# Kernel optimization log

Measured on AMD Instinct MI355X. Metric: run time of the kernel, lower is better.

The kernel has to match this reference:

```python
import jax, jax.numpy as jnp
import numpy as np

N_NODES = 100_000
N_EDGES = 1_000_000
IN_FTS = 64
EDGE_IN_FTS = 64
OUT_DIM = 64
LN_EPS = 1e-5


def setup_inputs() -> dict:
    key = jax.random.key(0)
    ks = jax.random.split(key, 9)
    def lin(k, fan_in, fan_out):
        bound = 1.0 / np.sqrt(fan_in)
        kw, kb = jax.random.split(k)
        W = jax.random.uniform(kw, (fan_out, fan_in), jnp.float32, -bound, bound)
        b = jax.random.uniform(kb, (fan_out,), jnp.float32, -bound, bound)
        return W, b
    node_fts = jax.random.normal(ks[0], (N_NODES, IN_FTS), jnp.float32)
    edge_fts = jax.random.normal(ks[1], (N_EDGES, EDGE_IN_FTS), jnp.float32)
    edges = jax.random.randint(ks[2], (2, N_EDGES), 0, N_NODES, jnp.int64)
    W_init, b_init = lin(ks[3], EDGE_IN_FTS, OUT_DIM)
    W_mlp, b_mlp = lin(ks[4], 2 * IN_FTS + OUT_DIM, OUT_DIM)
    W_alpha, b_alpha = lin(ks[5], 2 * IN_FTS + OUT_DIM, 1)
    return {
        "node_fts": node_fts, "edge_fts": edge_fts, "edges": edges,
        "W_init": W_init, "b_init": b_init,
        "W_mlp": W_mlp, "b_mlp": b_mlp,
        "W_alpha": W_alpha, "b_alpha": b_alpha,
    }


def _layer_norm(x):
    # F.layer_norm over last dim, no affine params
    m = jnp.mean(x, axis=-1, keepdims=True)
    v = jnp.mean(jnp.square(x - m), axis=-1, keepdims=True)
    return (x - m) * jax.lax.rsqrt(v + LN_EPS)


def reference(node_fts, edge_fts, edges, W_init, b_init, W_mlp, b_mlp, W_alpha, b_alpha):
    # initial edge projection: [E, edge_in] -> [E, out_dim]
    e = edge_fts @ W_init.T + b_init
    # gather head/tail node features: [E, in_fts] each
    head_vectors = jnp.take(node_fts, edges[0], axis=0)
    tail_vectors = jnp.take(node_fts, edges[1], axis=0)
    combined = jnp.concatenate([e, head_vectors, tail_vectors], axis=1)  # [E, 2*in+out]
    alpha = jax.nn.sigmoid(combined @ W_alpha.T + b_alpha)  # [E, 1]
    processed = jnp.tanh(combined @ W_mlp.T + b_mlp)        # [E, out_dim]
    right_side = _layer_norm(processed) * alpha
    return _layer_norm(e + right_side)
```

## Files before the change

### kernel.cpp

```cpp
#include <hip/hip_runtime.h>
#include <hip/hip_bf16.h>

typedef __bf16 bf16;
typedef bf16 bf16x8 __attribute__((ext_vector_type(8)));
typedef float f32x4 __attribute__((ext_vector_type(4)));

#define MFMA16(a, b, c) __builtin_amdgcn_mfma_f32_16x16x32_bf16((a), (b), (c), 0, 0, 0)

__device__ __forceinline__ float fast_rcp(float x) { return __builtin_amdgcn_rcpf(x); }
__device__ __forceinline__ float fast_rsq(float x) { return __builtin_amdgcn_rsqf(x); }
__device__ __forceinline__ float fast_tanh(float x) {
    float e = __expf(2.0f * x);
    return 1.0f - 2.0f * fast_rcp(e + 1.0f);
}
__device__ __forceinline__ float fast_sigmoid(float x) {
    return fast_rcp(1.0f + __expf(-x));
}

__device__ __forceinline__ bf16x8 cvt8(const float* __restrict__ p) {
    f32x4 a = *(const f32x4*)p;
    f32x4 b = *(const f32x4*)(p + 4);
    bf16x8 r;
    r[0] = (bf16)a[0]; r[1] = (bf16)a[1]; r[2] = (bf16)a[2]; r[3] = (bf16)a[3];
    r[4] = (bf16)b[0]; r[5] = (bf16)b[1]; r[6] = (bf16)b[2]; r[7] = (bf16)b[3];
    return r;
}

#define WS_WAF  8192
#define WS_BMF  8320
#define WS_BAF  8576

__global__ void fuse_weights_kernel(const float* __restrict__ W_init,
                                    const float* __restrict__ b_init,
                                    const float* __restrict__ W_mlp,
                                    const float* __restrict__ b_mlp,
                                    const float* __restrict__ W_alpha,
                                    const float* __restrict__ b_alpha,
                                    char* __restrict__ ws)
{
    bf16*  Wf  = (bf16*)ws;
    bf16*  waf = (bf16*)(ws + WS_WAF);
    float* bMf = (float*)(ws + WS_BMF);
    float* bAf = (float*)(ws + WS_BAF);
    const int idx = blockIdx.x * 256 + threadIdx.x;
    if (idx < 4096) {
        const int o = idx >> 6, k = idx & 63;
        float acc = 0.f;
        for (int j = 0; j < 64; ++j)
            acc += W_mlp[o * 192 + j] * W_init[j * 64 + k];
        Wf[o * 64 + k] = (bf16)acc;
    } else if (idx < 4160) {
        const int o = idx - 4096;
        float acc = b_mlp[o];
        for (int j = 0; j < 64; ++j)
            acc += W_mlp[o * 192 + j] * b_init[j];
        bMf[o] = acc;
    } else if (idx < 4224) {
        const int k = idx - 4160;
        float acc = 0.f;
        for (int j = 0; j < 64; ++j)
            acc += W_alpha[j] * W_init[j * 64 + k];
        waf[k] = (bf16)acc;
    } else if (idx == 4224) {
        float acc = b_alpha[0];
        for (int j = 0; j < 64; ++j)
            acc += W_alpha[j] * b_init[j];
        bAf[0] = acc;
    }
}

__global__ __launch_bounds__(256, 3)
void edge_update_kernel(const float* __restrict__ node_fts,
                        const float* __restrict__ edge_fts,
                        const int*   __restrict__ edges,
                        const float* __restrict__ W_init,
                        const float* __restrict__ b_init,
                        const float* __restrict__ W_mlp,
                        const float* __restrict__ W_alpha,
                        const char*  __restrict__ ws,
                        float* __restrict__ out,
                        int E)
{
    __shared__ bf16 sW2[64][200];
    __shared__ bf16 sWa[224];

    const int tid  = threadIdx.x;
    const int lane = tid & 63;
    const int wv   = tid >> 6;
    const int n    = lane & 15;
    const int q    = lane >> 4;

    const bf16*  Wf  = (const bf16*)ws;
    const bf16*  waf = (const bf16*)(ws + WS_WAF);
    const float* bMf = (const float*)(ws + WS_BMF);
    const float* bAf = (const float*)(ws + WS_BAF);

    for (int c = tid; c < 64 * 24; c += 256) {
        const int r = c / 24;
        const int o = (c - r * 24) * 8;
        if (o < 64) *(bf16x8*)(&sW2[r][o]) = *(const bf16x8*)(Wf + r * 64 + o);
        else        *(bf16x8*)(&sW2[r][o]) = cvt8(W_mlp + r * 192 + o);
    }
    if (tid < 24) {
        const int o = tid * 8;
        if (o < 64) *(bf16x8*)(&sWa[o]) = *(const bf16x8*)(waf + o);
        else        *(bf16x8*)(&sWa[o]) = cvt8(W_alpha + o);
    }
    __syncthreads();

    bf16x8 B1[2][4];
#pragma unroll
    for (int kk = 0; kk < 2; ++kk)
#pragma unroll
        for (int t = 0; t < 4; ++t)
            B1[kk][t] = cvt8(W_init + (t * 16 + n) * 64 + kk * 32 + q * 8);

    float bI[4], bM[4];
#pragma unroll
    for (int t = 0; t < 4; ++t) {
        bI[t] = b_init[t * 16 + n];
        bM[t] = bMf[t * 16 + n];
    }
    const float bA = bAf[0];

    const int ngroups = E >> 4;
    for (int g = blockIdx.x * 4 + wv; g < ngroups; g += gridDim.x * 4) {
        const int e0 = g << 4;
        const int h  = edges[e0 + n];
        const int tl = edges[E + e0 + n];

        bf16x8 A[6];
        A[0] = cvt8(edge_fts + (e0 + n) * 64 +      q * 8);
        A[1] = cvt8(edge_fts + (e0 + n) * 64 + 32 + q * 8);
        A[2] = cvt8(node_fts + h  * 64 +      q * 8);
        A[3] = cvt8(node_fts + h  * 64 + 32 + q * 8);
        A[4] = cvt8(node_fts + tl * 64 +      q * 8);
        A[5] = cvt8(node_fts + tl * 64 + 32 + q * 8);

        f32x4 accE[4] = { f32x4{0,0,0,0}, f32x4{0,0,0,0}, f32x4{0,0,0,0}, f32x4{0,0,0,0} };
#pragma unroll
        for (int kk = 0; kk < 2; ++kk)
#pragma unroll
            for (int t = 0; t < 4; ++t) accE[t] = MFMA16(A[kk], B1[kk][t], accE[t]);

        f32x4 accP[4] = { f32x4{0,0,0,0}, f32x4{0,0,0,0}, f32x4{0,0,0,0}, f32x4{0,0,0,0} };
        f32x4 accA = f32x4{0,0,0,0};
#pragma unroll
        for (int kk = 0; kk < 6; ++kk) {
            accA = MFMA16(A[kk], *(const bf16x8*)(&sWa[kk * 32 + q * 8]), accA);
#pragma unroll
            for (int t = 0; t < 4; ++t)
                accP[t] = MFMA16(A[kk], *(const bf16x8*)(&sW2[t * 16 + n][kk * 32 + q * 8]), accP[t]);
        }

        float eF[4][4], p[4][4], alpha[4];
#pragma unroll
        for (int t = 0; t < 4; ++t)
#pragma unroll
            for (int r = 0; r < 4; ++r) eF[t][r] = accE[t][r] + bI[t];
#pragma unroll
        for (int r = 0; r < 4; ++r) alpha[r] = fast_sigmoid(accA[r] + bA);
#pragma unroll
        for (int t = 0; t < 4; ++t)
#pragma unroll
            for (int r = 0; r < 4; ++r) p[t][r] = fast_tanh(accP[t][r] + bM[t]);

        float s1[4], s2[4];
#pragma unroll
        for (int r = 0; r < 4; ++r) {
            s1[r] = p[0][r] + p[1][r] + p[2][r] + p[3][r];
            s2[r] = p[0][r]*p[0][r] + p[1][r]*p[1][r] + p[2][r]*p[2][r] + p[3][r]*p[3][r];
        }
#pragma unroll
        for (int d = 1; d < 16; d <<= 1)
#pragma unroll
            for (int r = 0; r < 4; ++r) {
                s1[r] += __shfl_xor(s1[r], d, 64);
                s2[r] += __shfl_xor(s2[r], d, 64);
            }

        float o2[4][4];
#pragma unroll
        for (int r = 0; r < 4; ++r) {
            const float mean = s1[r] * 0.015625f;
            const float var  = fmaxf(s2[r] * 0.015625f - mean * mean, 0.0f);
            const float rs   = fast_rsq(var + 1e-5f);
#pragma unroll
            for (int t = 0; t < 4; ++t)
                o2[t][r] = eF[t][r] + (p[t][r] - mean) * rs * alpha[r];
        }

#pragma unroll
        for (int r = 0; r < 4; ++r) {
            s1[r] = o2[0][r] + o2[1][r] + o2[2][r] + o2[3][r];
            s2[r] = o2[0][r]*o2[0][r] + o2[1][r]*o2[1][r] + o2[2][r]*o2[2][r] + o2[3][r]*o2[3][r];
        }
#pragma unroll
        for (int d = 1; d < 16; d <<= 1)
#pragma unroll
            for (int r = 0; r < 4; ++r) {
                s1[r] += __shfl_xor(s1[r], d, 64);
                s2[r] += __shfl_xor(s2[r], d, 64);
            }
#pragma unroll
        for (int r = 0; r < 4; ++r) {
            const float mean = s1[r] * 0.015625f;
            const float var  = fmaxf(s2[r] * 0.015625f - mean * mean, 0.0f);
            const float rs   = fast_rsq(var + 1e-5f);
#pragma unroll
            for (int t = 0; t < 4; ++t)
                out[(e0 + q * 4 + r) * 64 + t * 16 + n] = (o2[t][r] - mean) * rs;
        }
    }
}

extern "C" void kernel_launch(void* const* d_in, const int* in_sizes, int n_in,
                              void* d_out, int out_size, void* d_ws, size_t ws_size,
                              hipStream_t stream) {
    const float* node_fts = (const float*)d_in[0];
    const float* edge_fts = (const float*)d_in[1];
    const int*   edges    = (const int*)d_in[2];
    const float* W_init   = (const float*)d_in[3];
    const float* b_init   = (const float*)d_in[4];
    const float* W_mlp    = (const float*)d_in[5];
    const float* b_mlp    = (const float*)d_in[6];
    const float* W_alpha  = (const float*)d_in[7];
    const float* b_alpha  = (const float*)d_in[8];
    float* out = (float*)d_out;
    char*  ws  = (char*)d_ws;

    const int E = in_sizes[2] / 2;

    hipLaunchKernelGGL(fuse_weights_kernel, dim3(17), dim3(256), 0, stream,
                       W_init, b_init, W_mlp, b_mlp, W_alpha, b_alpha, ws);
    hipLaunchKernelGGL(edge_update_kernel, dim3(2048), dim3(256), 0, stream,
                       node_fts, edge_fts, edges, W_init, b_init,
                       W_mlp, W_alpha, ws, out, E);
}
```

Measured before the change: 688.6 us.

## Pre-convert node features to bf16, double-buffer edge loads, DPP row reductions

A prep kernel now also converts node_fts to bf16 in the workspace, so the gathered head/tail rows are half as many bytes. The edge loop becomes a two-stage software pipeline that issues the next group's global loads and edge indices before computing the current group. W_init is moved into shared memory instead of being held in registers, and the cross-lane LayerNorm sums use DPP row shifts instead of shuffles. This adds a full pass over node_fts and more live registers for the prefetch buffers, which may reduce occupancy.

```diff
diff --git a/kernel.cpp b/kernel.cpp
--- a/kernel.cpp
+++ b/kernel.cpp
@@ -6,6 +6,7 @@
 typedef float f32x4 __attribute__((ext_vector_type(4)));
 
 #define MFMA16(a, b, c) __builtin_amdgcn_mfma_f32_16x16x32_bf16((a), (b), (c), 0, 0, 0)
+#define UNROLL _Pragma("unroll")
 
 __device__ __forceinline__ float fast_rcp(float x) { return __builtin_amdgcn_rcpf(x); }
 __device__ __forceinline__ float fast_rsq(float x) { return __builtin_amdgcn_rsqf(x); }
@@ -25,50 +26,111 @@
     r[4] = (bf16)b[0]; r[5] = (bf16)b[1]; r[6] = (bf16)b[2]; r[7] = (bf16)b[3];
     return r;
 }
+__device__ __forceinline__ bf16x8 cvt8v(f32x4 a, f32x4 b) {
+    bf16x8 r;
+    r[0] = (bf16)a[0]; r[1] = (bf16)a[1]; r[2] = (bf16)a[2]; r[3] = (bf16)a[3];
+    r[4] = (bf16)b[0]; r[5] = (bf16)b[1]; r[6] = (bf16)b[2]; r[7] = (bf16)b[3];
+    return r;
+}
+
+template <int CTRL>
+__device__ __forceinline__ float dpp_add(float v) {
+    int t = __builtin_amdgcn_update_dpp(0, __float_as_int(v), CTRL, 0xF, 0xF, false);
+    return v + __int_as_float(t);
+}
+__device__ __forceinline__ float sum16(float v) {
+    v = dpp_add<0x121>(v);
+    v = dpp_add<0x122>(v);
+    v = dpp_add<0x124>(v);
+    v = dpp_add<0x128>(v);
+    return v;
+}
 
 #define WS_WAF  8192
 #define WS_BMF  8320
 #define WS_BAF  8576
-
-__global__ void fuse_weights_kernel(const float* __restrict__ W_init,
-                                    const float* __restrict__ b_init,
-                                    const float* __restrict__ W_mlp,
-                                    const float* __restrict__ b_mlp,
-                                    const float* __restrict__ W_alpha,
-                                    const float* __restrict__ b_alpha,
-                                    char* __restrict__ ws)
+#define WS_NODE 16384
+
+__global__ void prep_kernel(const float* __restrict__ W_init,
+                            const float* __restrict__ b_init,
+                            const float* __restrict__ W_mlp,
+                            const float* __restrict__ b_mlp,
+                            const float* __restrict__ W_alpha,
+                            const float* __restrict__ b_alpha,
+                            const float* __restrict__ node_fts,
+                            char* __restrict__ ws,
+                            int nchunks)
 {
-    bf16*  Wf  = (bf16*)ws;
-    bf16*  waf = (bf16*)(ws + WS_WAF);
-    float* bMf = (float*)(ws + WS_BMF);
-    float* bAf = (float*)(ws + WS_BAF);
     const int idx = blockIdx.x * 256 + threadIdx.x;
-    if (idx < 4096) {
-        const int o = idx >> 6, k = idx & 63;
-        float acc = 0.f;
-        for (int j = 0; j < 64; ++j)
-            acc += W_mlp[o * 192 + j] * W_init[j * 64 + k];
-        Wf[o * 64 + k] = (bf16)acc;
-    } else if (idx < 4160) {
-        const int o = idx - 4096;
-        float acc = b_mlp[o];
-        for (int j = 0; j < 64; ++j)
-            acc += W_mlp[o * 192 + j] * b_init[j];
-        bMf[o] = acc;
-    } else if (idx < 4224) {
-        const int k = idx - 4160;
-        float acc = 0.f;
-        for (int j = 0; j < 64; ++j)
-            acc += W_alpha[j] * W_init[j * 64 + k];
-        waf[k] = (bf16)acc;
-    } else if (idx == 4224) {
-        float acc = b_alpha[0];
-        for (int j = 0; j < 64; ++j)
-            acc += W_alpha[j] * b_init[j];
-        bAf[0] = acc;
-    }
-}
-
+    if (blockIdx.x < 17) {
+        bf16*  Wf  = (bf16*)ws;
+        bf16*  waf = (bf16*)(ws + WS_WAF);
+        float* bMf = (float*)(ws + WS_BMF);
+        float* bAf = (float*)(ws + WS_BAF);
+        if (idx < 4096) {
+            const int o = idx >> 6, k = idx & 63;
+            float acc = 0.f;
+            for (int j = 0; j < 64; ++j)
+                acc += W_mlp[o * 192 + j] * W_init[j * 64 + k];
+            Wf[o * 64 + k] = (bf16)acc;
+        } else if (idx < 4160) {
+            const int o = idx - 4096;
+            float acc = b_mlp[o];
+            for (int j = 0; j < 64; ++j)
+                acc += W_mlp[o * 192 + j] * b_init[j];
+            bMf[o] = acc;
+        } else if (idx < 4224) {
+            const int k = idx - 4160;
+            float acc = 0.f;
+            for (int j = 0; j < 64; ++j)
+                acc += W_alpha[j] * W_init[j * 64 + k];
+            waf[k] = (bf16)acc;
+        } else if (idx == 4224) {
+            float acc = b_alpha[0];
+            for (int j = 0; j < 64; ++j)
+                acc += W_alpha[j] * b_init[j];
+            bAf[0] = acc;
+        }
+    } else {
+        const int i = idx - 17 * 256;
+        if (i < nchunks) {
+            bf16* nc = (bf16*)(ws + WS_NODE);
+            f32x4 a = *(const f32x4*)(node_fts + (size_t)i * 8);
+            f32x4 b = *(const f32x4*)(node_fts + (size_t)i * 8 + 4);
+            *(bf16x8*)(nc + (size_t)i * 8) = cvt8v(a, b);
+        }
+    }
+}
+
+#define ISSUE_STAGE(sp, e0s, hs, ts)                                          \
+    {                                                                         \
+        const float* ep_ = edge_fts + ((size_t)(e0s) + n) * 64;               \
+        ef[sp][0] = *(const f32x4*)(ep_ + q * 8);                             \
+        ef[sp][1] = *(const f32x4*)(ep_ + q * 8 + 4);                         \
+        ef[sp][2] = *(const f32x4*)(ep_ + 32 + q * 8);                        \
+        ef[sp][3] = *(const f32x4*)(ep_ + 32 + q * 8 + 4);                    \
+        if constexpr (NB) {                                                   \
+            const bf16* hp_ = nc + (size_t)(hs) * 64;                         \
+            const bf16* tp_ = nc + (size_t)(ts) * 64;                         \
+            nhB[sp][0] = *(const bf16x8*)(hp_ + q * 8);                       \
+            nhB[sp][1] = *(const bf16x8*)(hp_ + 32 + q * 8);                  \
+            ntB[sp][0] = *(const bf16x8*)(tp_ + q * 8);                       \
+            ntB[sp][1] = *(const bf16x8*)(tp_ + 32 + q * 8);                  \
+        } else {                                                              \
+            const float* hp_ = node_fts + (size_t)(hs) * 64;                  \
+            const float* tp_ = node_fts + (size_t)(ts) * 64;                  \
+            nhF[sp][0] = *(const f32x4*)(hp_ + q * 8);                        \
+            nhF[sp][1] = *(const f32x4*)(hp_ + q * 8 + 4);                    \
+            nhF[sp][2] = *(const f32x4*)(hp_ + 32 + q * 8);                   \
+            nhF[sp][3] = *(const f32x4*)(hp_ + 32 + q * 8 + 4);               \
+            ntF[sp][0] = *(const f32x4*)(tp_ + q * 8);                        \
+            ntF[sp][1] = *(const f32x4*)(tp_ + q * 8 + 4);                    \
+            ntF[sp][2] = *(const f32x4*)(tp_ + 32 + q * 8);                   \
+            ntF[sp][3] = *(const f32x4*)(tp_ + 32 + q * 8 + 4);               \
+        }                                                                     \
+    }
+
+template <bool NB>
 __global__ __launch_bounds__(256, 3)
 void edge_update_kernel(const float* __restrict__ node_fts,
                         const float* __restrict__ edge_fts,
@@ -81,7 +143,7 @@
                         float* __restrict__ out,
                         int E)
 {
-    __shared__ bf16 sW2[64][200];
+    __shared__ bf16 sW2[64][264];
     __shared__ bf16 sWa[224];
 
     const int tid  = threadIdx.x;
@@ -94,12 +156,14 @@
     const bf16*  waf = (const bf16*)(ws + WS_WAF);
     const float* bMf = (const float*)(ws + WS_BMF);
     const float* bAf = (const float*)(ws + WS_BAF);
-
-    for (int c = tid; c < 64 * 24; c += 256) {
-        const int r = c / 24;
-        const int o = (c - r * 24) * 8;
-        if (o < 64) *(bf16x8*)(&sW2[r][o]) = *(const bf16x8*)(Wf + r * 64 + o);
-        else        *(bf16x8*)(&sW2[r][o]) = cvt8(W_mlp + r * 192 + o);
+    const bf16*  nc  = (const bf16*)(ws + WS_NODE);
+
+    for (int c = tid; c < 64 * 33; c += 256) {
+        const int r = c / 33;
+        const int o = (c - r * 33) * 8;
+        if (o < 64)       *(bf16x8*)(&sW2[r][o]) = *(const bf16x8*)(Wf + r * 64 + o);
+        else if (o < 192) *(bf16x8*)(&sW2[r][o]) = cvt8(W_mlp + r * 192 + o);
+        else if (o < 256) *(bf16x8*)(&sW2[r][o]) = cvt8(W_init + r * 64 + (o - 192));
     }
     if (tid < 24) {
         const int o = tid * 8;
@@ -108,15 +172,8 @@
     }
     __syncthreads();
 
-    bf16x8 B1[2][4];
-#pragma unroll
-    for (int kk = 0; kk < 2; ++kk)
-#pragma unroll
-        for (int t = 0; t < 4; ++t)
-            B1[kk][t] = cvt8(W_init + (t * 16 + n) * 64 + kk * 32 + q * 8);
-
     float bI[4], bM[4];
-#pragma unroll
+    UNROLL
     for (int t = 0; t < 4; ++t) {
         bI[t] = b_init[t * 16 + n];
         bM[t] = bMf[t * 16 + n];
@@ -124,92 +181,133 @@
     const float bA = bAf[0];
 
     const int ngroups = E >> 4;
-    for (int g = blockIdx.x * 4 + wv; g < ngroups; g += gridDim.x * 4) {
-        const int e0 = g << 4;
-        const int h  = edges[e0 + n];
-        const int tl = edges[E + e0 + n];
-
-        bf16x8 A[6];
-        A[0] = cvt8(edge_fts + (e0 + n) * 64 +      q * 8);
-        A[1] = cvt8(edge_fts + (e0 + n) * 64 + 32 + q * 8);
-        A[2] = cvt8(node_fts + h  * 64 +      q * 8);
-        A[3] = cvt8(node_fts + h  * 64 + 32 + q * 8);
-        A[4] = cvt8(node_fts + tl * 64 +      q * 8);
-        A[5] = cvt8(node_fts + tl * 64 + 32 + q * 8);
-
-        f32x4 accE[4] = { f32x4{0,0,0,0}, f32x4{0,0,0,0}, f32x4{0,0,0,0}, f32x4{0,0,0,0} };
-#pragma unroll
-        for (int kk = 0; kk < 2; ++kk)
-#pragma unroll
-            for (int t = 0; t < 4; ++t) accE[t] = MFMA16(A[kk], B1[kk][t], accE[t]);
-
-        f32x4 accP[4] = { f32x4{0,0,0,0}, f32x4{0,0,0,0}, f32x4{0,0,0,0}, f32x4{0,0,0,0} };
-        f32x4 accA = f32x4{0,0,0,0};
-#pragma unroll
-        for (int kk = 0; kk < 6; ++kk) {
-            accA = MFMA16(A[kk], *(const bf16x8*)(&sWa[kk * 32 + q * 8]), accA);
-#pragma unroll
+    const int stride  = gridDim.x * 4;
+    int gc = blockIdx.x * 4 + wv;
+    if (gc >= ngroups) return;
+
+    f32x4  ef[2][4];
+    bf16x8 nhB[2][2], ntB[2][2];
+    f32x4  nhF[2][4], ntF[2][4];
+
+    {
+        const int e0 = gc << 4;
+        const int hc = edges[e0 + n];
+        const int tc = edges[E + e0 + n];
+        ISSUE_STAGE(0, e0, hc, tc);
+    }
+    int gn = gc + stride, hn = 0, tn = 0;
+    if (gn < ngroups) {
+        const int e0n = gn << 4;
+        hn = edges[e0n + n];
+        tn = edges[E + e0n + n];
+    } else {
+        gn = gc;
+    }
+
+    for (;;) {
+        UNROLL
+        for (int p = 0; p < 2; ++p) {
+            const int np = p ^ 1;
+            const bool haveNext = (gn != gc);
+            int g2 = gn;
+            if (haveNext) {
+                ISSUE_STAGE(np, gn << 4, hn, tn);
+                g2 = gn + stride;
+                if (g2 < ngroups) {
+                    const int e2 = g2 << 4;
+                    hn = edges[e2 + n];
+                    tn = edges[E + e2 + n];
+                } else {
+                    g2 = gn;
+                }
+            }
+
+            const int e0c = gc << 4;
+            bf16x8 A[6];
+            A[0] = cvt8v(ef[p][0], ef[p][1]);
+            A[1] = cvt8v(ef[p][2], ef[p][3]);
+            if constexpr (NB) {
+                A[2] = nhB[p][0]; A[3] = nhB[p][1];
+                A[4] = ntB[p][0]; A[5] = ntB[p][1];
+            } else {
+                A[2] = cvt8v(nhF[p][0], nhF[p][1]); A[3] = cvt8v(nhF[p][2], nhF[p][3]);
+                A[4] = cvt8v(ntF[p][0], ntF[p][1]); A[5] = cvt8v(ntF[p][2], ntF[p][3]);
+            }
+
+            f32x4 accE[4] = { f32x4{0,0,0,0}, f32x4{0,0,0,0}, f32x4{0,0,0,0}, f32x4{0,0,0,0} };
+            UNROLL
+            for (int kk = 0; kk < 2; ++kk)
+                UNROLL
+                for (int t = 0; t < 4; ++t)
+                    accE[t] = MFMA16(A[kk],
+                                     *(const bf16x8*)(&sW2[t * 16 + n][192 + kk * 32 + q * 8]),
+                                     accE[t]);
+
+            f32x4 accP[4] = { f32x4{0,0,0,0}, f32x4{0,0,0,0}, f32x4{0,0,0,0}, f32x4{0,0,0,0} };
+            f32x4 accA = f32x4{0,0,0,0};
+            UNROLL
+            for (int kk = 0; kk < 6; ++kk) {
+                accA = MFMA16(A[kk], *(const bf16x8*)(&sWa[kk * 32 + q * 8]), accA);
+                UNROLL
+                for (int t = 0; t < 4; ++t)
+                    accP[t] = MFMA16(A[kk],
+                                     *(const bf16x8*)(&sW2[t * 16 + n][kk * 32 + q * 8]),
+                                     accP[t]);
+            }
+
+            float eF[4][4], pv[4][4], alpha[4];
+            UNROLL
             for (int t = 0; t < 4; ++t)
-                accP[t] = MFMA16(A[kk], *(const bf16x8*)(&sW2[t * 16 + n][kk * 32 + q * 8]), accP[t]);
-        }
-
-        float eF[4][4], p[4][4], alpha[4];
-#pragma unroll
-        for (int t = 0; t < 4; ++t)
-#pragma unroll
-            for (int r = 0; r < 4; ++r) eF[t][r] = accE[t][r] + bI[t];
-#pragma unroll
-        for (int r = 0; r < 4; ++r) alpha[r] = fast_sigmoid(accA[r] + bA);
-#pragma unroll
-        for (int t = 0; t < 4; ++t)
-#pragma unroll
-            for (int r = 0; r < 4; ++r) p[t][r] = fast_tanh(accP[t][r] + bM[t]);
-
-        float s1[4], s2[4];
-#pragma unroll
-        for (int r = 0; r < 4; ++r) {
-            s1[r] = p[0][r] + p[1][r] + p[2][r] + p[3][r];
-            s2[r] = p[0][r]*p[0][r] + p[1][r]*p[1][r] + p[2][r]*p[2][r] + p[3][r]*p[3][r];
-        }
-#pragma unroll
-        for (int d = 1; d < 16; d <<= 1)
-#pragma unroll
+                UNROLL
+                for (int r = 0; r < 4; ++r) eF[t][r] = accE[t][r] + bI[t];
+            UNROLL
+            for (int r = 0; r < 4; ++r) alpha[r] = fast_sigmoid(accA[r] + bA);
+            UNROLL
+            for (int t = 0; t < 4; ++t)
+                UNROLL
+                for (int r = 0; r < 4; ++r) pv[t][r] = fast_tanh(accP[t][r] + bM[t]);
+
+            float s1[4], s2[4];
+            UNROLL
             for (int r = 0; r < 4; ++r) {
-                s1[r] += __shfl_xor(s1[r], d, 64);
-                s2[r] += __shfl_xor(s2[r], d, 64);
-            }
-
-        float o2[4][4];
-#pragma unroll
-        for (int r = 0; r < 4; ++r) {
-            const float mean = s1[r] * 0.015625f;
-            const float var  = fmaxf(s2[r] * 0.015625f - mean * mean, 0.0f);
-            const float rs   = fast_rsq(var + 1e-5f);
-#pragma unroll
-            for (int t = 0; t < 4; ++t)
-                o2[t][r] = eF[t][r] + (p[t][r] - mean) * rs * alpha[r];
-        }
-
-#pragma unroll
-        for (int r = 0; r < 4; ++r) {
-            s1[r] = o2[0][r] + o2[1][r] + o2[2][r] + o2[3][r];
-            s2[r] = o2[0][r]*o2[0][r] + o2[1][r]*o2[1][r] + o2[2][r]*o2[2][r] + o2[3][r]*o2[3][r];
-        }
-#pragma unroll
-        for (int d = 1; d < 16; d <<= 1)
-#pragma unroll
+                s1[r] = pv[0][r] + pv[1][r] + pv[2][r] + pv[3][r];
+                s2[r] = pv[0][r]*pv[0][r] + pv[1][r]*pv[1][r] + pv[2][r]*pv[2][r] + pv[3][r]*pv[3][r];
+            }
+            UNROLL
+            for (int r = 0; r < 4; ++r) { s1[r] = sum16(s1[r]); s2[r] = sum16(s2[r]); }
+
+            float o2[4][4];
+            UNROLL
             for (int r = 0; r < 4; ++r) {
-                s1[r] += __shfl_xor(s1[r], d, 64);
-                s2[r] += __shfl_xor(s2[r], d, 64);
-            }
-#pragma unroll
-        for (int r = 0; r < 4; ++r) {
-            const float mean = s1[r] * 0.015625f;
-            const float var  = fmaxf(s2[r] * 0.015625f - mean * mean, 0.0f);
-            const float rs   = fast_rsq(var + 1e-5f);
-#pragma unroll
-            for (int t = 0; t < 4; ++t)
-                out[(e0 + q * 4 + r) * 64 + t * 16 + n] = (o2[t][r] - mean) * rs;
+                const float mean = s1[r] * 0.015625f;
+                const float var  = fmaxf(s2[r] * 0.015625f - mean * mean, 0.0f);
+                const float rs   = fast_rsq(var + 1e-5f);
+                UNROLL
+                for (int t = 0; t < 4; ++t)
+                    o2[t][r] = eF[t][r] + (pv[t][r] - mean) * rs * alpha[r];
+            }
+
+            UNROLL
+            for (int r = 0; r < 4; ++r) {
+                s1[r] = o2[0][r] + o2[1][r] + o2[2][r] + o2[3][r];
+                s2[r] = o2[0][r]*o2[0][r] + o2[1][r]*o2[1][r] + o2[2][r]*o2[2][r] + o2[3][r]*o2[3][r];
+            }
+            UNROLL
+            for (int r = 0; r < 4; ++r) { s1[r] = sum16(s1[r]); s2[r] = sum16(s2[r]); }
+
+            UNROLL
+            for (int r = 0; r < 4; ++r) {
+                const float mean = s1[r] * 0.015625f;
+                const float var  = fmaxf(s2[r] * 0.015625f - mean * mean, 0.0f);
+                const float rs   = fast_rsq(var + 1e-5f);
+                UNROLL
+                for (int t = 0; t < 4; ++t)
+                    out[((size_t)e0c + q * 4 + r) * 64 + t * 16 + n] = (o2[t][r] - mean) * rs;
+            }
+
+            if (!haveNext) return;
+            gc = gn;
+            gn = g2;
         }
     }
 }
@@ -230,10 +328,24 @@
     char*  ws  = (char*)d_ws;
 
     const int E = in_sizes[2] / 2;
-
-    hipLaunchKernelGGL(fuse_weights_kernel, dim3(17), dim3(256), 0, stream,
-                       W_init, b_init, W_mlp, b_mlp, W_alpha, b_alpha, ws);
-    hipLaunchKernelGGL(edge_update_kernel, dim3(2048), dim3(256), 0, stream,
-                       node_fts, edge_fts, edges, W_init, b_init,
-                       W_mlp, W_alpha, ws, out, E);
-}
+    const int N = in_sizes[0] / 64;
+
+    const size_t need = (size_t)WS_NODE + (size_t)N * 64 * 2;
+    const bool   nb   = ws_size >= need;
+    const int    nchunks = N * 8;
+
+    const int prep_blocks = nb ? (17 + (nchunks + 255) / 256) : 17;
+    hipLaunchKernelGGL(prep_kernel, dim3(prep_blocks), dim3(256), 0, stream,
+                       W_init, b_init, W_mlp, b_mlp, W_alpha, b_alpha,
+                       node_fts, ws, nb ? nchunks : 0);
+
+    if (nb) {
+        hipLaunchKernelGGL((edge_update_kernel<true>), dim3(2048), dim3(256), 0, stream,
+                           node_fts, edge_fts, edges, W_init, b_init,
+                           W_mlp, W_alpha, ws, out, E);
+    } else {
+        hipLaunchKernelGGL((edge_update_kernel<false>), dim3(2048), dim3(256), 0, stream,
+                           node_fts, edge_fts, edges, W_init, b_init,
+                           W_mlp, W_alpha, ws, out, E);
+    }
+}
```

Result: no change. 695.3 us (+1.0%).
